# Performance work log

Hardware: AMD Instinct MI355X
Metric: run time of the kernel (lower is better)

## Reference

```python
import jax, jax.numpy as jnp
import numpy as np

D = 64
H = 4
FF = 4  # fourier features
EPS = 1e-5


def _ln(x, g, b):
    m = jnp.mean(x, axis=-1, keepdims=True)
    v = jnp.mean((x - m) ** 2, axis=-1, keepdims=True)
    return (x - m) / jnp.sqrt(v + EPS) * g + b


def setup_inputs() -> dict:
    key = jax.random.key(0)
    ks = jax.random.split(key, 30)
    s = 0.05
    inp = {
        'feats': jax.random.normal(ks[0], (1, 1024, D), jnp.float32),
        'coors': jax.random.normal(ks[1], (1, 1024, 3), jnp.float32),
        'qkv_w': jax.random.normal(ks[2], (D, 3 * D), jnp.float32) * s,
        'out_w': jax.random.normal(ks[3], (D, D), jnp.float32) * s,
        'out_b': jnp.zeros((D,), jnp.float32),
        'edge_w1': jax.random.normal(ks[4], (2 * FF + 1, D), jnp.float32) * s,
        'edge_b1': jnp.zeros((D,), jnp.float32),
        'edge_w2': jax.random.normal(ks[5], (D, D), jnp.float32) * s,
        'edge_b2': jnp.zeros((D,), jnp.float32),
        'coord_w1': jax.random.normal(ks[6], (D, D), jnp.float32) * s,
        'coord_b1': jnp.zeros((D,), jnp.float32),
        'coord_w2': jax.random.normal(ks[7], (D, 1), jnp.float32) * s,
        'coord_b2': jnp.zeros((1,), jnp.float32),
        'gate_w1': jax.random.normal(ks[8], (D, D), jnp.float32) * s,
        'gate_b1': jnp.zeros((D,), jnp.float32),
        'gate_w2': jax.random.normal(ks[9], (D, 1), jnp.float32) * s,
        'gate_b2': jnp.zeros((1,), jnp.float32),
        'ln1_g': jnp.ones((D,), jnp.float32),
        'ln1_b': jnp.zeros((D,), jnp.float32),
        'ln2_g': jnp.ones((D,), jnp.float32),
        'ln2_b': jnp.zeros((D,), jnp.float32),
        'ffn_w1': jax.random.normal(ks[10], (D, 4 * D), jnp.float32) * s,
        'ffn_b1': jnp.zeros((4 * D,), jnp.float32),
        'ffn_w2': jax.random.normal(ks[11], (4 * D, D), jnp.float32) * s,
        'ffn_b2': jnp.zeros((D,), jnp.float32),
    }
    return inp


def reference(feats, coors, qkv_w, out_w, out_b, edge_w1, edge_b1, edge_w2, edge_b2,
              coord_w1, coord_b1, coord_w2, coord_b2, gate_w1, gate_b1, gate_w2, gate_b2,
              ln1_g, ln1_b, ln2_g, ln2_b, ffn_w1, ffn_b1, ffn_w2, ffn_b2):
    B, N, Dm = feats.shape
    x = _ln(feats, ln1_g, ln1_b)  # norm1 (pre-norm; also used as residual base, faithful to source)

    # pairwise relative coords and squared distance
    rel = coors[:, :, None, :] - coors[:, None, :, :]        # [B,N,N,3]
    rd = jnp.sum(rel ** 2, axis=-1, keepdims=True)            # [B,N,N,1]
    freqs = 2.0 ** jnp.arange(FF, dtype=coors.dtype)
    fr = rd / freqs                                           # [B,N,N,FF]
    enc = jnp.concatenate([jnp.sin(fr), jnp.cos(fr), rd], -1) # [B,N,N,2*FF+1]

    # edge MLP (edges=None, edge_dim=0)
    e_ij = jax.nn.silu(enc @ edge_w1 + edge_b1) @ edge_w2 + edge_b2  # [B,N,N,D]

    # attention
    qkv = x @ qkv_w
    q, k, v = jnp.split(qkv, 3, axis=-1)
    hd = Dm // H
    q = q.reshape(B, N, H, hd).transpose(0, 2, 1, 3)
    k = k.reshape(B, N, H, hd).transpose(0, 2, 1, 3)
    v = v.reshape(B, N, H, hd).transpose(0, 2, 1, 3)
    scores = jnp.einsum('bhid,bhjd->bhij', q, k) / jnp.sqrt(jnp.asarray(Dm, q.dtype))
    attn = jax.nn.softmax(scores, axis=-1)                    # [B,H,N,N]
    msg = jnp.einsum('bhij,bhjd->bhid', attn, v)
    msg = msg.transpose(0, 2, 1, 3).reshape(B, N, Dm)
    x = x + (msg @ out_w + out_b)
    x = x + (jax.nn.gelu(_ln(x, ln2_g, ln2_b) @ ffn_w1 + ffn_b1, approximate=False) @ ffn_w2 + ffn_b2)

    # coordinate update
    cw = (jax.nn.silu(e_ij @ coord_w1 + coord_b1) @ coord_w2 + coord_b2)[..., 0]  # [B,N,N]
    cw = cw * jnp.mean(attn, axis=1)
    gate = jax.nn.sigmoid(jax.nn.silu(x @ gate_w1 + gate_b1) @ gate_w2 + gate_b2)  # [B,N,1]
    delta = jnp.einsum('bij,bijd->bid', cw, rel) * gate
    return x, coors + delta
```

## Files before the change

kernel.cpp:

```cpp
#include <hip/hip_runtime.h>
#include <hip/hip_bf16.h>

#define N 1024
#define D 64

typedef __attribute__((ext_vector_type(8))) short bf16x8;
typedef __attribute__((ext_vector_type(4))) float f32x4;

__device__ __forceinline__ unsigned short f2b(float v) {
  unsigned u = __float_as_uint(v);
  u += 0x7fffu + ((u >> 16) & 1u);
  return (unsigned short)(u >> 16);
}
__device__ __forceinline__ unsigned short f2bc(float v) {
  union { __hip_bfloat16 h; unsigned short u; } r;
  r.h = __float2bfloat16(v);
  return r.u;
}
__device__ __forceinline__ unsigned pk2(float a, float b) {
  union { __hip_bfloat162 h; unsigned u; } r;
  r.h = __hip_bfloat162(__float2bfloat16(a), __float2bfloat16(b));
  return r.u;
}
__device__ __forceinline__ float bu(unsigned short u) {
  return __uint_as_float(((unsigned)u) << 16);
}
__device__ __forceinline__ float silu_f(float x) {
  return x * __builtin_amdgcn_rcpf(1.f + __expf(-x));
}
__device__ __forceinline__ float sigm_f(float x) {
  return __builtin_amdgcn_rcpf(1.f + __expf(-x));
}

__global__ __launch_bounds__(64) void k_ln1_qkv(
    const float* __restrict__ feats, const float* __restrict__ g, const float* __restrict__ b,
    const float* __restrict__ qkv_w, float* __restrict__ xn, float* __restrict__ qkv) {
  const int i = blockIdx.x, t = threadIdx.x;
  float v = feats[i * D + t];
  float s = v;
#pragma unroll
  for (int off = 32; off; off >>= 1) s += __shfl_xor(s, off);
  const float m = s * (1.0f / 64.0f);
  const float dv = v - m;
  float vs = dv * dv;
#pragma unroll
  for (int off = 32; off; off >>= 1) vs += __shfl_xor(vs, off);
  const float var = vs * (1.0f / 64.0f);
  const float xv = dv * rsqrtf(var + 1e-5f) * g[t] + b[t];
  xn[i * D + t] = xv;
  __shared__ float xs[D];
  xs[t] = xv;
  __syncthreads();
#pragma unroll
  for (int c = 0; c < 3; ++c) {
    const int col = t + c * 64;
    float acc = 0.f;
#pragma unroll 8
    for (int k = 0; k < D; ++k) acc += xs[k] * qkv_w[k * 192 + col];
    qkv[i * 192 + col] = acc;
  }
}

__global__ __launch_bounds__(256) void k_scores(
    const float* __restrict__ qkv, unsigned short* __restrict__ P,
    float* __restrict__ l_ws, float* __restrict__ pv_ws) {
  const int i0 = blockIdx.x * 64, j0 = blockIdx.y * 64, jb = blockIdx.y;
  const int t = threadIdx.x;
  const int lane = t & 63, h = t >> 6;
  const int l15 = lane & 15, lg = lane >> 4;
  const int r7 = l15 & 7;

  __shared__ __align__(16) unsigned short Qs[64 * 64];
  __shared__ __align__(16) unsigned short Ks[64 * 64];
  __shared__ __align__(16) unsigned short VTs[4 * 16 * 64];
  __shared__ __align__(16) unsigned short Ps[4 * 64 * 64];

  {
    const int si = t >> 2, q4 = t & 3;
    const int g0 = ((q4 * 2) ^ (si & 7)) * 8, g1 = ((q4 * 2 + 1) ^ (si & 7)) * 8;
    {
      const float* qr = &qkv[(i0 + si) * 192 + q4 * 16];
      float4 a0 = *(const float4*)(qr + 0), a1 = *(const float4*)(qr + 4);
      float4 a2 = *(const float4*)(qr + 8), a3 = *(const float4*)(qr + 12);
      *(uint4*)&Qs[si * 64 + g0] = make_uint4(
          pk2(a0.x * 0.125f, a0.y * 0.125f), pk2(a0.z * 0.125f, a0.w * 0.125f),
          pk2(a1.x * 0.125f, a1.y * 0.125f), pk2(a1.z * 0.125f, a1.w * 0.125f));
      *(uint4*)&Qs[si * 64 + g1] = make_uint4(
          pk2(a2.x * 0.125f, a2.y * 0.125f), pk2(a2.z * 0.125f, a2.w * 0.125f),
          pk2(a3.x * 0.125f, a3.y * 0.125f), pk2(a3.z * 0.125f, a3.w * 0.125f));
    }
    {
      const float* kr = &qkv[(j0 + si) * 192 + 64 + q4 * 16];
      float4 a0 = *(const float4*)(kr + 0), a1 = *(const float4*)(kr + 4);
      float4 a2 = *(const float4*)(kr + 8), a3 = *(const float4*)(kr + 12);
      *(uint4*)&Ks[si * 64 + g0] = make_uint4(pk2(a0.x, a0.y), pk2(a0.z, a0.w),
                                              pk2(a1.x, a1.y), pk2(a1.z, a1.w));
      *(uint4*)&Ks[si * 64 + g1] = make_uint4(pk2(a2.x, a2.y), pk2(a2.z, a2.w),
                                              pk2(a3.x, a3.y), pk2(a3.z, a3.w));
    }
    {
      const float* vr = &qkv[(j0 + si) * 192 + 128 + q4 * 16];
      float4 v0 = *(const float4*)(vr + 0), v1 = *(const float4*)(vr + 4);
      float4 v2 = *(const float4*)(vr + 8), v3 = *(const float4*)(vr + 12);
      float vv[16] = {v0.x, v0.y, v0.z, v0.w, v1.x, v1.y, v1.z, v1.w,
                      v2.x, v2.y, v2.z, v2.w, v3.x, v3.y, v3.z, v3.w};
      const int sj3 = si >> 3, sj7 = si & 7;
#pragma unroll
      for (int cc = 0; cc < 16; ++cc)
        VTs[q4 * 1024 + cc * 64 + ((sj3 ^ (cc & 7)) * 8) + sj7] = f2bc(vv[cc]);
    }
  }
  __syncthreads();

  const bf16x8 z8 = {0, 0, 0, 0, 0, 0, 0, 0};
  const int gk = ((h * 2 + (lg & 1)) ^ r7) * 8;
  bf16x8 qa[4], kb[4];
#pragma unroll
  for (int it = 0; it < 4; ++it) {
    qa[it] = *(const bf16x8*)&Qs[(it * 16 + l15) * 64 + gk];
    if (lg >= 2) qa[it] = z8;
    kb[it] = *(const bf16x8*)&Ks[(it * 16 + l15) * 64 + gk];
  }
  f32x4 acc[4][4];
#pragma unroll
  for (int it = 0; it < 4; ++it)
#pragma unroll
    for (int jt = 0; jt < 4; ++jt)
      acc[it][jt] = (f32x4){0.f, 0.f, 0.f, 0.f};
#pragma unroll
  for (int it = 0; it < 4; ++it)
#pragma unroll
    for (int jt = 0; jt < 4; ++jt)
      acc[it][jt] = __builtin_amdgcn_mfma_f32_16x16x32_bf16(qa[it], kb[jt], acc[it][jt], 0, 0, 0);

  float prow[4][4];
#pragma unroll
  for (int it = 0; it < 4; ++it)
#pragma unroll
    for (int rr = 0; rr < 4; ++rr) prow[it][rr] = 0.f;
#pragma unroll
  for (int it = 0; it < 4; ++it)
#pragma unroll
    for (int jt = 0; jt < 4; ++jt)
#pragma unroll
      for (int rr = 0; rr < 4; ++rr) {
        const float p = __expf(acc[it][jt][rr]);
        prow[it][rr] += p;
        const int irow = it * 16 + lg * 4 + rr;
        const int col = jt * 16 + l15;
        Ps[h * 4096 + irow * 64 + (((col >> 3) ^ (irow & 7)) * 8) + (col & 7)] = f2bc(p);
      }
#pragma unroll
  for (int it = 0; it < 4; ++it)
#pragma unroll
    for (int rr = 0; rr < 4; ++rr) {
      float s = prow[it][rr];
      s += __shfl_xor(s, 1); s += __shfl_xor(s, 2);
      s += __shfl_xor(s, 4); s += __shfl_xor(s, 8);
      if (l15 == 0)
        l_ws[h * 16384 + jb * 1024 + i0 + it * 16 + lg * 4 + rr] = s;
    }

  f32x4 av[4];
#pragma unroll
  for (int it = 0; it < 4; ++it) av[it] = (f32x4){0.f, 0.f, 0.f, 0.f};
#pragma unroll
  for (int ks = 0; ks < 2; ++ks) {
    const int gj = ((ks * 4 + lg) ^ r7) * 8;
    bf16x8 vb = *(const bf16x8*)&VTs[h * 1024 + l15 * 64 + gj];
#pragma unroll
    for (int it = 0; it < 4; ++it) {
      bf16x8 pa = *(const bf16x8*)&Ps[h * 4096 + (it * 16 + l15) * 64 + gj];
      av[it] = __builtin_amdgcn_mfma_f32_16x16x32_bf16(pa, vb, av[it], 0, 0, 0);
    }
  }
#pragma unroll
  for (int it = 0; it < 4; ++it)
#pragma unroll
    for (int rr = 0; rr < 4; ++rr)
      pv_ws[jb * 65536 + (i0 + it * 16 + lg * 4 + rr) * 64 + h * 16 + l15] = av[it][rr];

  {
    const int ir = t & 63;
    unsigned short* pg = &P[h * 1048576 + (i0 + ir) * 1024 + j0];
#pragma unroll
    for (int gg = 0; gg < 8; ++gg)
      *(uint4*)&pg[gg * 8] = *(const uint4*)&Ps[h * 4096 + ir * 64 + ((gg ^ (ir & 7)) * 8)];
  }
}

__global__ __launch_bounds__(256) void k_meanattn(
    const unsigned short* P, const float* __restrict__ l_ws,
    unsigned short* ma, unsigned short* __restrict__ maT) {
  const int i0 = blockIdx.x * 64, j0 = blockIdx.y * 64;
  const int t = threadIdx.x;
  __shared__ float invl[4][64];
  __shared__ unsigned short tile[64][68];
  {
    const int h = t >> 6, r = t & 63;
    float s = 0.f;
#pragma unroll
    for (int jt = 0; jt < 16; ++jt) s += l_ws[h * 16384 + jt * 1024 + i0 + r];
    invl[h][r] = 0.25f * __builtin_amdgcn_rcpf(s);
  }
  __syncthreads();
  {
    const int r = t >> 2, cg = t & 3;
    float v[16];
#pragma unroll
    for (int k = 0; k < 16; ++k) v[k] = 0.f;
#pragma unroll
    for (int h = 0; h < 4; ++h) {
      const unsigned short* pr = &P[h * 1048576 + (i0 + r) * 1024 + j0 + cg * 16];
      uint4 a = *(const uint4*)pr;
      uint4 b2 = *(const uint4*)(pr + 8);
      const float sh = invl[h][r];
      unsigned uu[8] = {a.x, a.y, a.z, a.w, b2.x, b2.y, b2.z, b2.w};
#pragma unroll
      for (int q = 0; q < 8; ++q) {
        v[q * 2 + 0] += sh * bu((unsigned short)(uu[q] & 0xffffu));
        v[q * 2 + 1] += sh * bu((unsigned short)(uu[q] >> 16));
      }
    }
    unsigned out[8];
#pragma unroll
    for (int q = 0; q < 8; ++q) out[q] = pk2(v[2 * q], v[2 * q + 1]);
    unsigned short* mr = &ma[(i0 + r) * 1024 + j0 + cg * 16];
    *(uint4*)mr = make_uint4(out[0], out[1], out[2], out[3]);
    *(uint4*)(mr + 8) = make_uint4(out[4], out[5], out[6], out[7]);
#pragma unroll
    for (int q = 0; q < 8; ++q) {
      tile[r][cg * 16 + 2 * q] = (unsigned short)(out[q] & 0xffffu);
      tile[r][cg * 16 + 2 * q + 1] = (unsigned short)(out[q] >> 16);
    }
  }
  __syncthreads();
  {
    const int jr = t >> 2, icg = t & 3;
    unsigned out[8];
#pragma unroll
    for (int q = 0; q < 8; ++q) {
      const unsigned short lo = tile[icg * 16 + 2 * q][jr];
      const unsigned short hi = tile[icg * 16 + 2 * q + 1][jr];
      out[q] = (unsigned)lo | ((unsigned)hi << 16);
    }
    unsigned short* mtr = &maT[(j0 + jr) * 1024 + i0 + icg * 16];
    *(uint4*)mtr = make_uint4(out[0], out[1], out[2], out[3]);
    *(uint4*)(mtr + 8) = make_uint4(out[4], out[5], out[6], out[7]);
  }
}

__global__ __launch_bounds__(256) void k_ffn_gate(
    const float* __restrict__ pv_ws, const float* __restrict__ l_ws,
    const float* __restrict__ xn,
    const float* __restrict__ out_w, const float* __restrict__ out_b,
    const float* __restrict__ ln2_g, const float* __restrict__ ln2_b,
    const float* __restrict__ fw1, const float* __restrict__ fb1,
    const float* __restrict__ fw2, const float* __restrict__ fb2,
    const float* __restrict__ gw1, const float* __restrict__ gb1,
    const float* __restrict__ gw2, const float* __restrict__ gb2,
    float* __restrict__ xout, float* __restrict__ gate) {
  const int i = blockIdx.x, t = threadIdx.x;
  __shared__ float msgv[64], xs[64], x1s[64], hs[256];
  if (t < 64) {
    float ls = 0.f;
#pragma unroll
    for (int jt = 0; jt < 16; ++jt) ls += l_ws[(t >> 4) * 16384 + jt * 1024 + i];
    const float invh = __builtin_amdgcn_rcpf(ls);
    float s = 0.f;
#pragma unroll
    for (int jt = 0; jt < 16; ++jt) s += pv_ws[jt * 65536 + i * 64 + t];
    msgv[t] = s * invh;
  }
  __syncthreads();
  if (t < 64) {
    float o = out_b[t];
#pragma unroll 8
    for (int k = 0; k < 64; ++k) o += msgv[k] * out_w[k * 64 + t];
    const float v = xn[i * 64 + t] + o;
    x1s[t] = v;
    float s = v;
#pragma unroll
    for (int off = 32; off; off >>= 1) s += __shfl_xor(s, off);
    const float m = s * (1.f / 64.f);
    const float dv = v - m;
    float vs = dv * dv;
#pragma unroll
    for (int off = 32; off; off >>= 1) vs += __shfl_xor(vs, off);
    xs[t] = dv * rsqrtf(vs * (1.f / 64.f) + 1e-5f) * ln2_g[t] + ln2_b[t];
  }
  __syncthreads();
  float a = fb1[t];
#pragma unroll 8
  for (int k = 0; k < 64; ++k) a += xs[k] * fw1[k * 256 + t];
  const float ge = 0.5f * a * (1.f + erff(a * 0.70710678118f));
  hs[t] = ge;
  __syncthreads();
  if (t < 64) {
    float o = fb2[t];
#pragma unroll 8
    for (int k = 0; k < 256; ++k) o += hs[k] * fw2[k * 64 + t];
    const float xo = x1s[t] + o;
    xout[i * 64 + t] = xo;
    xs[t] = xo;
  }
  __syncthreads();
  if (t < 64) {
    float a2 = gb1[t];
#pragma unroll 8
    for (int k = 0; k < 64; ++k) a2 += xs[k] * gw1[k * 64 + t];
    const float sg = a2 * sigm_f(a2);
    float pp = sg * gw2[t];
#pragma unroll
    for (int off = 32; off; off >>= 1) pp += __shfl_xor(pp, off);
    if (t == 0) gate[i] = sigm_f(pp + gb2[0]);
  }
}

__global__ __launch_bounds__(256) void k_prep(
    const float* __restrict__ ew1, const float* __restrict__ eb1,
    const float* __restrict__ ew2, const float* __restrict__ cw1,
    const float* __restrict__ eb2, const float* __restrict__ cb1,
    unsigned short* __restrict__ pw, float* __restrict__ b3p) {
  const int t = threadIdx.x;
  __shared__ float wc[64][64];
  for (int idx = t; idx < 4096; idx += 256) {
    const int r = idx >> 6, c = idx & 63;
    float s = 0.f;
#pragma unroll 8
    for (int k = 0; k < 64; ++k) s += ew2[r * 64 + k] * cw1[k * 64 + c];
    wc[r][c] = s;
  }
  __syncthreads();
  for (int idx = t; idx < 12 * 512; idx += 256) {
    const int e = idx & 7, l = (idx >> 3) & 63, f = idx >> 9;
    const int l15 = l & 15, lg = l >> 4;
    float v;
    if (f < 4) {
      const int d = f * 16 + l15, k = lg * 8 + e;
      v = (k < 9) ? ew1[k * 64 + d] : (k == 9 ? eb1[d] : 0.f);
    } else {
      const int g = f - 4, d = (g >> 1) * 16 + l15, k = (g & 1) * 32 + lg * 8 + e;
      v = wc[k][d];
    }
    pw[idx] = f2b(v);
  }
  if (t < 64) {
    float s = cb1[t];
#pragma unroll 8
    for (int k = 0; k < 64; ++k) s += eb2[k] * cw1[k * 64 + t];
    b3p[t] = s;
  }
}

__global__ __launch_bounds__(256, 2) void k_pair(
    const float* __restrict__ coors,
    const unsigned short* __restrict__ ma, const unsigned short* __restrict__ maT,
    const unsigned short* __restrict__ pw,
    const float* __restrict__ b3p, const float* __restrict__ c2g,
    const float* __restrict__ cb2, float* __restrict__ partial) {
  int bb = blockIdx.x, ti = 0;
  while (bb >= 32 - ti) { bb -= 32 - ti; ++ti; }
  const int tj = ti + bb;
  const bool diag = (ti == tj);
  const int nch = diag ? 4 : 8;

  const int t = threadIdx.x;
  const int w = t >> 6;
  const int lane = t & 63;
  const int l15 = lane & 15;
  const int lg = lane >> 4;

  __shared__ __align__(16) unsigned short buf[4][32][64];
  __shared__ float4 relA[4][32], relB[4][32];
  __shared__ float di[4][32][3], dj[4][32][3];

  bf16x8 wf[12];
#pragma unroll
  for (int f = 0; f < 12; ++f)
    wf[f] = *(const bf16x8*)&pw[(f * 64 + lane) * 8];

  float b3v[16], c2v[16];
#pragma unroll
  for (int mt = 0; mt < 4; ++mt)
#pragma unroll
    for (int r = 0; r < 4; ++r) {
      const int d = mt * 16 + lg * 4 + r;
      b3v[mt * 4 + r] = b3p[d];
      c2v[mt * 4 + r] = c2g[d];
    }
  const float cb2q = cb2[0] * 0.25f;

  if (lane < 32) {
    const int j = lane;
#pragma unroll
    for (int k2 = 0; k2 < 3; ++k2) { di[w][j][k2] = 0.f; dj[w][j][k2] = 0.f; }
    unsigned short* rp = &buf[w][j][0];
    const uint4 z4 = make_uint4(0, 0, 0, 0);
    *(uint4*)&rp[(1 ^ (j & 7)) * 8] = z4;
    *(uint4*)&rp[(2 ^ (j & 7)) * 8] = z4;
    *(uint4*)&rp[(3 ^ (j & 7)) * 8] = z4;
  }

  f32x4 acc[4][2];

  for (int c = 0; c < nch; ++c) {
    const int dgn = diag ? (c * 4 + w + 1) : (c * 4 + w);
    {
      const int p = lane & 31;
      const int hhalf = lane >> 5;
      const int ig = ti * 32 + p;
      const int jj = (p + dgn) & 31;
      const int jg = tj * 32 + jj;
      const float rx = coors[ig * 3 + 0] - coors[jg * 3 + 0];
      const float ry = coors[ig * 3 + 1] - coors[jg * 3 + 1];
      const float rz = coors[ig * 3 + 2] - coors[jg * 3 + 2];
      const float rd = rx * rx + ry * ry + rz * rz;
      unsigned short* rp = &buf[w][p][0];
      if (hhalf == 0) {
        float mi = bu(ma[ig * 1024 + jg]);
        float mj = bu(maT[ig * 1024 + jg]);
        if (diag && dgn == 16 && p >= 16) { mi = 0.f; mj = 0.f; }
        relA[w][p] = make_float4(mi * rx, mi * ry, mi * rz, 0.f);
        relB[w][p] = make_float4(mj * rx, mj * ry, mj * rz, 0.f);
        *(uint2*)&rp[(0 ^ (p & 7)) * 8] =
            make_uint2(pk2(__sinf(rd), __sinf(rd * 0.5f)),
                       pk2(__sinf(rd * 0.25f), __sinf(rd * 0.125f)));
        *(unsigned*)&rp[(1 ^ (p & 7)) * 8] = pk2(rd, 1.0f);
      } else {
        *(uint2*)&rp[((0 ^ (p & 7)) * 8) + 4] =
            make_uint2(pk2(__cosf(rd), __cosf(rd * 0.5f)),
                       pk2(__cosf(rd * 0.25f), __cosf(rd * 0.125f)));
      }
    }

#pragma unroll
    for (int mt = 0; mt < 4; ++mt)
#pragma unroll
      for (int nt = 0; nt < 2; ++nt)
        acc[mt][nt] = (f32x4){0.f, 0.f, 0.f, 0.f};
    {
      const int j0 = l15, j1 = 16 + l15;
      bf16x8 bf0 = *(const bf16x8*)&buf[w][j0][(lg ^ (j0 & 7)) * 8];
      bf16x8 bf1 = *(const bf16x8*)&buf[w][j1][(lg ^ (j1 & 7)) * 8];
#pragma unroll
      for (int mt = 0; mt < 4; ++mt) {
        acc[mt][0] = __builtin_amdgcn_mfma_f32_16x16x32_bf16(wf[mt], bf0, acc[mt][0], 0, 0, 0);
        acc[mt][1] = __builtin_amdgcn_mfma_f32_16x16x32_bf16(wf[mt], bf1, acc[mt][1], 0, 0, 0);
      }
    }
#pragma unroll
    for (int mt = 0; mt < 4; ++mt)
#pragma unroll
      for (int nt = 0; nt < 2; ++nt) {
        const f32x4 a = acc[mt][nt];
        const unsigned lo = pk2(silu_f(a[0]), silu_f(a[1]));
        const unsigned hi = pk2(silu_f(a[2]), silu_f(a[3]));
        const int j = nt * 16 + l15;
        const int g = mt * 2 + (lg >> 1);
        *(uint2*)&buf[w][j][((g ^ (j & 7)) * 8) + (lg & 1) * 4] = make_uint2(lo, hi);
      }

#pragma unroll
    for (int mt = 0; mt < 4; ++mt)
#pragma unroll
      for (int nt = 0; nt < 2; ++nt)
        acc[mt][nt] = (f32x4){b3v[mt * 4 + 0], b3v[mt * 4 + 1], b3v[mt * 4 + 2], b3v[mt * 4 + 3]};
#pragma unroll
    for (int ks = 0; ks < 2; ++ks) {
      const int gi = ks * 4 + lg;
      const int j0 = l15, j1 = 16 + l15;
      bf16x8 bf0 = *(const bf16x8*)&buf[w][j0][(gi ^ (j0 & 7)) * 8];
      bf16x8 bf1 = *(const bf16x8*)&buf[w][j1][(gi ^ (j1 & 7)) * 8];
#pragma unroll
      for (int mt = 0; mt < 4; ++mt) {
        acc[mt][0] = __builtin_amdgcn_mfma_f32_16x16x32_bf16(wf[4 + mt * 2 + ks], bf0, acc[mt][0], 0, 0, 0);
        acc[mt][1] = __builtin_amdgcn_mfma_f32_16x16x32_bf16(wf[4 + mt * 2 + ks], bf1, acc[mt][1], 0, 0, 0);
      }
    }

#pragma unroll
    for (int nt = 0; nt < 2; ++nt) {
      float cwp = cb2q;
#pragma unroll
      for (int mt = 0; mt < 4; ++mt) {
        const f32x4 a = acc[mt][nt];
#pragma unroll
        for (int r = 0; r < 4; ++r) cwp += silu_f(a[r]) * c2v[mt * 4 + r];
      }
      cwp += __shfl_xor(cwp, 16);
      cwp += __shfl_xor(cwp, 32);
      if (lg == 0) {
        const int p = nt * 16 + l15;
        const int jj = (p + dgn) & 31;
        const float4 rA = relA[w][p];
        const float4 rB = relB[w][p];
        di[w][p][0] += cwp * rA.x; di[w][p][1] += cwp * rA.y; di[w][p][2] += cwp * rA.z;
        dj[w][jj][0] -= cwp * rB.x; dj[w][jj][1] -= cwp * rB.y; dj[w][jj][2] -= cwp * rB.z;
      }
    }
  }

  __syncthreads();
  if (!diag) {
    if (t < 96) {
      const int p = t / 3, k = t % 3;
      const float s = di[0][p][k] + di[1][p][k] + di[2][p][k] + di[3][p][k];
      partial[tj * 3072 + (ti * 32 + p) * 3 + k] = s;
    } else if (t < 192) {
      const int u = t - 96, q = u / 3, k = u % 3;
      const float s = dj[0][q][k] + dj[1][q][k] + dj[2][q][k] + dj[3][q][k];
      partial[ti * 3072 + (tj * 32 + q) * 3 + k] = s;
    }
  } else {
    if (t < 96) {
      const int p = t / 3, k = t % 3;
      const float s = di[0][p][k] + di[1][p][k] + di[2][p][k] + di[3][p][k]
                    + dj[0][p][k] + dj[1][p][k] + dj[2][p][k] + dj[3][p][k];
      partial[ti * 3072 + (ti * 32 + p) * 3 + k] = s;
    }
  }
}

__global__ __launch_bounds__(256) void k_finalize(
    const float* __restrict__ coors, const float* __restrict__ partial,
    const float* __restrict__ gate, float* __restrict__ outc) {
  const int idx = blockIdx.x * 256 + threadIdx.x;
  if (idx < 3072) {
    float s = 0.f;
#pragma unroll
    for (int sl = 0; sl < 32; ++sl) s += partial[sl * 3072 + idx];
    outc[idx] = coors[idx] + s * gate[idx / 3];
  }
}

extern "C" void kernel_launch(void* const* d_in, const int* in_sizes, int n_in,
                              void* d_out, int out_size, void* d_ws, size_t ws_size,
                              hipStream_t stream) {
  const float* feats = (const float*)d_in[0];
  const float* coors = (const float*)d_in[1];
  const float* qkv_w = (const float*)d_in[2];
  const float* out_w = (const float*)d_in[3];
  const float* out_b = (const float*)d_in[4];
  const float* ew1 = (const float*)d_in[5];
  const float* eb1 = (const float*)d_in[6];
  const float* ew2 = (const float*)d_in[7];
  const float* eb2 = (const float*)d_in[8];
  const float* cw1 = (const float*)d_in[9];
  const float* cb1 = (const float*)d_in[10];
  const float* cw2 = (const float*)d_in[11];
  const float* cb2 = (const float*)d_in[12];
  const float* gw1 = (const float*)d_in[13];
  const float* gb1 = (const float*)d_in[14];
  const float* gw2 = (const float*)d_in[15];
  const float* gb2 = (const float*)d_in[16];
  const float* ln1_g = (const float*)d_in[17];
  const float* ln1_b = (const float*)d_in[18];
  const float* ln2_g = (const float*)d_in[19];
  const float* ln2_b = (const float*)d_in[20];
  const float* fw1 = (const float*)d_in[21];
  const float* fb1 = (const float*)d_in[22];
  const float* fw2 = (const float*)d_in[23];
  const float* fb2 = (const float*)d_in[24];

  float* ws = (float*)d_ws;
  float* xn = ws;
  float* qkv = ws + 65536;
  float* gate = ws + 262144;
  unsigned short* pw = (unsigned short*)(ws + 263168);
  float* b3p = ws + 266240;
  float* l_ws = ws + 266304;
  float* pv_ws = ws + 331840;
  float* partial = ws + 1380416;
  unsigned short* P = (unsigned short*)(ws + 1478720);
  unsigned short* ma = P;
  unsigned short* maT = (unsigned short*)(ws + 3575872);

  float* xout = (float*)d_out;
  float* coorout = xout + 65536;

  hipLaunchKernelGGL(k_ln1_qkv, dim3(N), dim3(64), 0, stream, feats, ln1_g, ln1_b, qkv_w, xn, qkv);
  hipLaunchKernelGGL(k_prep, dim3(1), dim3(256), 0, stream, ew1, eb1, ew2, cw1, eb2, cb1, pw, b3p);
  hipLaunchKernelGGL(k_scores, dim3(16, 16), dim3(256), 0, stream, qkv, P, l_ws, pv_ws);
  hipLaunchKernelGGL(k_meanattn, dim3(16, 16), dim3(256), 0, stream, P, l_ws, ma, maT);
  hipLaunchKernelGGL(k_ffn_gate, dim3(N), dim3(256), 0, stream, pv_ws, l_ws, xn,
                     out_w, out_b, ln2_g, ln2_b,
                     fw1, fb1, fw2, fb2, gw1, gb1, gw2, gb2, xout, gate);
  hipLaunchKernelGGL(k_pair, dim3(528), dim3(256), 0, stream, coors, ma, maT, pw,
                     b3p, cw2, cb2, partial);
  hipLaunchKernelGGL(k_finalize, dim3(12), dim3(256), 0, stream, coors, partial, gate, coorout);
}
```

Before: 105.2 us.

## Drop transposed mean-attention buffer and shrink pair tiles to 16x16

Removes the maT transpose output from k_meanattn, eliminating its shared-memory tile, a barrier and a full N×N bf16 write. k_pair now reads the transposed entry directly from ma at [jg, ig], which is a strided, uncoalesced gather. The pair kernel's triangular tiling changes from 32-row tiles (528 blocks) to 16-row tiles (2080 blocks) with fewer diagonal iterations per block, so finalize now sums 64 partial slices. The finer grid improves load balance and occupancy, at the cost of more per-block setup such as weight fragment loads and zeroing.

```diff
diff --git a/kernel.cpp b/kernel.cpp
--- a/kernel.cpp
+++ b/kernel.cpp
@@ -190,12 +190,10 @@
 }
 
 __global__ __launch_bounds__(256) void k_meanattn(
-    const unsigned short* P, const float* __restrict__ l_ws,
-    unsigned short* ma, unsigned short* __restrict__ maT) {
+    const unsigned short* P, const float* __restrict__ l_ws, unsigned short* ma) {
   const int i0 = blockIdx.x * 64, j0 = blockIdx.y * 64;
   const int t = threadIdx.x;
   __shared__ float invl[4][64];
-  __shared__ unsigned short tile[64][68];
   {
     const int h = t >> 6, r = t & 63;
     float s = 0.f;
@@ -228,25 +226,6 @@
     unsigned short* mr = &ma[(i0 + r) * 1024 + j0 + cg * 16];
     *(uint4*)mr = make_uint4(out[0], out[1], out[2], out[3]);
     *(uint4*)(mr + 8) = make_uint4(out[4], out[5], out[6], out[7]);
-#pragma unroll
-    for (int q = 0; q < 8; ++q) {
-      tile[r][cg * 16 + 2 * q] = (unsigned short)(out[q] & 0xffffu);
-      tile[r][cg * 16 + 2 * q + 1] = (unsigned short)(out[q] >> 16);
-    }
-  }
-  __syncthreads();
-  {
-    const int jr = t >> 2, icg = t & 3;
-    unsigned out[8];
-#pragma unroll
-    for (int q = 0; q < 8; ++q) {
-      const unsigned short lo = tile[icg * 16 + 2 * q][jr];
-      const unsigned short hi = tile[icg * 16 + 2 * q + 1][jr];
-      out[q] = (unsigned)lo | ((unsigned)hi << 16);
-    }
-    unsigned short* mtr = &maT[(j0 + jr) * 1024 + i0 + icg * 16];
-    *(uint4*)mtr = make_uint4(out[0], out[1], out[2], out[3]);
-    *(uint4*)(mtr + 8) = make_uint4(out[4], out[5], out[6], out[7]);
   }
 }
 
@@ -354,16 +333,15 @@
 }
 
 __global__ __launch_bounds__(256, 2) void k_pair(
-    const float* __restrict__ coors,
-    const unsigned short* __restrict__ ma, const unsigned short* __restrict__ maT,
+    const float* __restrict__ coors, const unsigned short* __restrict__ ma,
     const unsigned short* __restrict__ pw,
     const float* __restrict__ b3p, const float* __restrict__ c2g,
     const float* __restrict__ cb2, float* __restrict__ partial) {
   int bb = blockIdx.x, ti = 0;
-  while (bb >= 32 - ti) { bb -= 32 - ti; ++ti; }
+  while (bb >= 64 - ti) { bb -= 64 - ti; ++ti; }
   const int tj = ti + bb;
   const bool diag = (ti == tj);
-  const int nch = diag ? 4 : 8;
+  const int niter = diag ? 1 : 2;
 
   const int t = threadIdx.x;
   const int w = t >> 6;
@@ -373,7 +351,7 @@
 
   __shared__ __align__(16) unsigned short buf[4][32][64];
   __shared__ float4 relA[4][32], relB[4][32];
-  __shared__ float di[4][32][3], dj[4][32][3];
+  __shared__ float di[4][16][3], dj[4][16][3];
 
   bf16x8 wf[12];
 #pragma unroll
@@ -393,42 +371,45 @@
 
   if (lane < 32) {
     const int j = lane;
-#pragma unroll
-    for (int k2 = 0; k2 < 3; ++k2) { di[w][j][k2] = 0.f; dj[w][j][k2] = 0.f; }
     unsigned short* rp = &buf[w][j][0];
     const uint4 z4 = make_uint4(0, 0, 0, 0);
     *(uint4*)&rp[(1 ^ (j & 7)) * 8] = z4;
     *(uint4*)&rp[(2 ^ (j & 7)) * 8] = z4;
     *(uint4*)&rp[(3 ^ (j & 7)) * 8] = z4;
   }
+  if (lane < 16) {
+#pragma unroll
+    for (int k2 = 0; k2 < 3; ++k2) { di[w][lane][k2] = 0.f; dj[w][lane][k2] = 0.f; }
+  }
 
   f32x4 acc[4][2];
 
-  for (int c = 0; c < nch; ++c) {
-    const int dgn = diag ? (c * 4 + w + 1) : (c * 4 + w);
+  for (int c = 0; c < niter; ++c) {
+    const int d0 = diag ? (1 + w * 2) : ((w + c * 4) * 2);
     {
-      const int p = lane & 31;
+      const int cc = lane & 31;
       const int hhalf = lane >> 5;
-      const int ig = ti * 32 + p;
-      const int jj = (p + dgn) & 31;
-      const int jg = tj * 32 + jj;
+      const int p = cc & 15;
+      const int dd = d0 + (cc >> 4);
+      const int ig = ti * 16 + p;
+      const int jg = tj * 16 + ((p + dd) & 15);
       const float rx = coors[ig * 3 + 0] - coors[jg * 3 + 0];
       const float ry = coors[ig * 3 + 1] - coors[jg * 3 + 1];
       const float rz = coors[ig * 3 + 2] - coors[jg * 3 + 2];
       const float rd = rx * rx + ry * ry + rz * rz;
-      unsigned short* rp = &buf[w][p][0];
+      unsigned short* rp = &buf[w][cc][0];
       if (hhalf == 0) {
         float mi = bu(ma[ig * 1024 + jg]);
-        float mj = bu(maT[ig * 1024 + jg]);
-        if (diag && dgn == 16 && p >= 16) { mi = 0.f; mj = 0.f; }
-        relA[w][p] = make_float4(mi * rx, mi * ry, mi * rz, 0.f);
-        relB[w][p] = make_float4(mj * rx, mj * ry, mj * rz, 0.f);
-        *(uint2*)&rp[(0 ^ (p & 7)) * 8] =
+        float mj = bu(ma[jg * 1024 + ig]);
+        if (diag && dd == 8 && p >= 8) { mi = 0.f; mj = 0.f; }
+        relA[w][cc] = make_float4(mi * rx, mi * ry, mi * rz, 0.f);
+        relB[w][cc] = make_float4(mj * rx, mj * ry, mj * rz, 0.f);
+        *(uint2*)&rp[(0 ^ (cc & 7)) * 8] =
             make_uint2(pk2(__sinf(rd), __sinf(rd * 0.5f)),
                        pk2(__sinf(rd * 0.25f), __sinf(rd * 0.125f)));
-        *(unsigned*)&rp[(1 ^ (p & 7)) * 8] = pk2(rd, 1.0f);
+        *(unsigned*)&rp[(1 ^ (cc & 7)) * 8] = pk2(rd, 1.0f);
       } else {
-        *(uint2*)&rp[((0 ^ (p & 7)) * 8) + 4] =
+        *(uint2*)&rp[((0 ^ (cc & 7)) * 8) + 4] =
             make_uint2(pk2(__cosf(rd), __cosf(rd * 0.5f)),
                        pk2(__cosf(rd * 0.25f), __cosf(rd * 0.125f)));
       }
@@ -491,10 +472,12 @@
       cwp += __shfl_xor(cwp, 16);
       cwp += __shfl_xor(cwp, 32);
       if (lg == 0) {
-        const int p = nt * 16 + l15;
-        const int jj = (p + dgn) & 31;
-        const float4 rA = relA[w][p];
-        const float4 rB = relB[w][p];
+        const int cc = nt * 16 + l15;
+        const int p = l15;
+        const int dd = d0 + nt;
+        const int jj = (p + dd) & 15;
+        const float4 rA = relA[w][cc];
+        const float4 rB = relB[w][cc];
         di[w][p][0] += cwp * rA.x; di[w][p][1] += cwp * rA.y; di[w][p][2] += cwp * rA.z;
         dj[w][jj][0] -= cwp * rB.x; dj[w][jj][1] -= cwp * rB.y; dj[w][jj][2] -= cwp * rB.z;
       }
@@ -503,21 +486,21 @@
 
   __syncthreads();
   if (!diag) {
-    if (t < 96) {
+    if (t < 48) {
       const int p = t / 3, k = t % 3;
       const float s = di[0][p][k] + di[1][p][k] + di[2][p][k] + di[3][p][k];
-      partial[tj * 3072 + (ti * 32 + p) * 3 + k] = s;
-    } else if (t < 192) {
-      const int u = t - 96, q = u / 3, k = u % 3;
+      partial[tj * 3072 + (ti * 16 + p) * 3 + k] = s;
+    } else if (t < 96) {
+      const int u = t - 48, q = u / 3, k = u % 3;
       const float s = dj[0][q][k] + dj[1][q][k] + dj[2][q][k] + dj[3][q][k];
-      partial[ti * 3072 + (tj * 32 + q) * 3 + k] = s;
+      partial[ti * 3072 + (tj * 16 + q) * 3 + k] = s;
     }
   } else {
-    if (t < 96) {
+    if (t < 48) {
       const int p = t / 3, k = t % 3;
       const float s = di[0][p][k] + di[1][p][k] + di[2][p][k] + di[3][p][k]
                     + dj[0][p][k] + dj[1][p][k] + dj[2][p][k] + dj[3][p][k];
-      partial[ti * 3072 + (ti * 32 + p) * 3 + k] = s;
+      partial[ti * 3072 + (ti * 16 + p) * 3 + k] = s;
     }
   }
 }
@@ -529,7 +512,7 @@
   if (idx < 3072) {
     float s = 0.f;
 #pragma unroll
-    for (int sl = 0; sl < 32; ++sl) s += partial[sl * 3072 + idx];
+    for (int sl = 0; sl < 64; ++sl) s += partial[sl * 3072 + idx];
     outc[idx] = coors[idx] + s * gate[idx / 3];
   }
 }
@@ -572,9 +555,8 @@
   float* l_ws = ws + 266304;
   float* pv_ws = ws + 331840;
   float* partial = ws + 1380416;
-  unsigned short* P = (unsigned short*)(ws + 1478720);
+  unsigned short* P = (unsigned short*)(ws + 1577024);
   unsigned short* ma = P;
-  unsigned short* maT = (unsigned short*)(ws + 3575872);
 
   float* xout = (float*)d_out;
   float* coorout = xout + 65536;
@@ -582,11 +564,11 @@
   hipLaunchKernelGGL(k_ln1_qkv, dim3(N), dim3(64), 0, stream, feats, ln1_g, ln1_b, qkv_w, xn, qkv);
   hipLaunchKernelGGL(k_prep, dim3(1), dim3(256), 0, stream, ew1, eb1, ew2, cw1, eb2, cb1, pw, b3p);
   hipLaunchKernelGGL(k_scores, dim3(16, 16), dim3(256), 0, stream, qkv, P, l_ws, pv_ws);
-  hipLaunchKernelGGL(k_meanattn, dim3(16, 16), dim3(256), 0, stream, P, l_ws, ma, maT);
+  hipLaunchKernelGGL(k_meanattn, dim3(16, 16), dim3(256), 0, stream, P, l_ws, ma);
   hipLaunchKernelGGL(k_ffn_gate, dim3(N), dim3(256), 0, stream, pv_ws, l_ws, xn,
                      out_w, out_b, ln2_g, ln2_b,
                      fw1, fb1, fw2, fb2, gw1, gb1, gw2, gb2, xout, gate);
-  hipLaunchKernelGGL(k_pair, dim3(528), dim3(256), 0, stream, coors, ma, maT, pw,
+  hipLaunchKernelGGL(k_pair, dim3(2080), dim3(256), 0, stream, coors, ma, pw,
                      b3p, cw2, cb2, partial);
   hipLaunchKernelGGL(k_finalize, dim3(12), dim3(256), 0, stream, coors, partial, gate, coorout);
 }
```

Result: slower. 111.8 us (+6.2%).

## Merge prep into LN/QKV kernel, drop transposed mean-attn, widen pair blocks

Applied to the files above, without the earlier changes.

The weight-prep kernel is folded into the LN1+QKV kernel as an extra block, and LN1+QKV now handles four rows per 256-thread block, which removes one launch. The transposed mean-attention matrix is no longer written; k_pair reads ma with transposed indexing instead, which saves a write pass but makes those loads strided. k_pair now runs with 512 threads (8 waves) that each do fewer iterations. The cb2 scaling changes from cb2*0.25 to cb2, presumably because the work split per block changed, which carries a correctness risk.

```diff
diff --git a/kernel.cpp b/kernel.cpp
--- a/kernel.cpp
+++ b/kernel.cpp
@@ -32,11 +32,49 @@
   return __builtin_amdgcn_rcpf(1.f + __expf(-x));
 }
 
-__global__ __launch_bounds__(64) void k_ln1_qkv(
+__global__ __launch_bounds__(256) void k_ln1_qkv_prep(
     const float* __restrict__ feats, const float* __restrict__ g, const float* __restrict__ b,
-    const float* __restrict__ qkv_w, float* __restrict__ xn, float* __restrict__ qkv) {
-  const int i = blockIdx.x, t = threadIdx.x;
-  float v = feats[i * D + t];
+    const float* __restrict__ qkv_w, float* __restrict__ xn, float* __restrict__ qkv,
+    const float* __restrict__ ew1, const float* __restrict__ eb1,
+    const float* __restrict__ ew2, const float* __restrict__ cw1,
+    const float* __restrict__ eb2, const float* __restrict__ cb1,
+    unsigned short* __restrict__ pw, float* __restrict__ b3p) {
+  __shared__ float sh[64 * 64];
+  const int t = threadIdx.x;
+  if (blockIdx.x == 256) {
+    float* wc = sh;
+    for (int idx = t; idx < 4096; idx += 256) {
+      const int r = idx >> 6, c = idx & 63;
+      float s = 0.f;
+#pragma unroll 8
+      for (int k = 0; k < 64; ++k) s += ew2[r * 64 + k] * cw1[k * 64 + c];
+      wc[idx] = s;
+    }
+    __syncthreads();
+    for (int idx = t; idx < 12 * 512; idx += 256) {
+      const int e = idx & 7, l = (idx >> 3) & 63, f = idx >> 9;
+      const int l15 = l & 15, lg = l >> 4;
+      float v;
+      if (f < 4) {
+        const int d = f * 16 + l15, k = lg * 8 + e;
+        v = (k < 9) ? ew1[k * 64 + d] : (k == 9 ? eb1[d] : 0.f);
+      } else {
+        const int gq = f - 4, d = (gq >> 1) * 16 + l15, k = (gq & 1) * 32 + lg * 8 + e;
+        v = wc[k * 64 + d];
+      }
+      pw[idx] = f2b(v);
+    }
+    if (t < 64) {
+      float s = cb1[t];
+#pragma unroll 8
+      for (int k = 0; k < 64; ++k) s += eb2[k] * cw1[k * 64 + t];
+      b3p[t] = s;
+    }
+    return;
+  }
+  const int r = t >> 6, lane = t & 63;
+  const int i = blockIdx.x * 4 + r;
+  float v = feats[i * D + lane];
   float s = v;
 #pragma unroll
   for (int off = 32; off; off >>= 1) s += __shfl_xor(s, off);
@@ -46,17 +84,17 @@
 #pragma unroll
   for (int off = 32; off; off >>= 1) vs += __shfl_xor(vs, off);
   const float var = vs * (1.0f / 64.0f);
-  const float xv = dv * rsqrtf(var + 1e-5f) * g[t] + b[t];
-  xn[i * D + t] = xv;
-  __shared__ float xs[D];
-  xs[t] = xv;
+  const float xv = dv * rsqrtf(var + 1e-5f) * g[lane] + b[lane];
+  xn[i * D + lane] = xv;
+  float* xs = sh;
+  xs[r * 64 + lane] = xv;
   __syncthreads();
 #pragma unroll
   for (int c = 0; c < 3; ++c) {
-    const int col = t + c * 64;
+    const int col = lane + c * 64;
     float acc = 0.f;
 #pragma unroll 8
-    for (int k = 0; k < D; ++k) acc += xs[k] * qkv_w[k * 192 + col];
+    for (int k = 0; k < D; ++k) acc += xs[r * 64 + k] * qkv_w[k * 192 + col];
     qkv[i * 192 + col] = acc;
   }
 }
@@ -190,12 +228,10 @@
 }
 
 __global__ __launch_bounds__(256) void k_meanattn(
-    const unsigned short* P, const float* __restrict__ l_ws,
-    unsigned short* ma, unsigned short* __restrict__ maT) {
+    const unsigned short* P, const float* __restrict__ l_ws, unsigned short* ma) {
   const int i0 = blockIdx.x * 64, j0 = blockIdx.y * 64;
   const int t = threadIdx.x;
   __shared__ float invl[4][64];
-  __shared__ unsigned short tile[64][68];
   {
     const int h = t >> 6, r = t & 63;
     float s = 0.f;
@@ -228,25 +264,6 @@
     unsigned short* mr = &ma[(i0 + r) * 1024 + j0 + cg * 16];
     *(uint4*)mr = make_uint4(out[0], out[1], out[2], out[3]);
     *(uint4*)(mr + 8) = make_uint4(out[4], out[5], out[6], out[7]);
-#pragma unroll
-    for (int q = 0; q < 8; ++q) {
-      tile[r][cg * 16 + 2 * q] = (unsigned short)(out[q] & 0xffffu);
-      tile[r][cg * 16 + 2 * q + 1] = (unsigned short)(out[q] >> 16);
-    }
-  }
-  __syncthreads();
-  {
-    const int jr = t >> 2, icg = t & 3;
-    unsigned out[8];
-#pragma unroll
-    for (int q = 0; q < 8; ++q) {
-      const unsigned short lo = tile[icg * 16 + 2 * q][jr];
-      const unsigned short hi = tile[icg * 16 + 2 * q + 1][jr];
-      out[q] = (unsigned)lo | ((unsigned)hi << 16);
-    }
-    unsigned short* mtr = &maT[(j0 + jr) * 1024 + i0 + icg * 16];
-    *(uint4*)mtr = make_uint4(out[0], out[1], out[2], out[3]);
-    *(uint4*)(mtr + 8) = make_uint4(out[4], out[5], out[6], out[7]);
   }
 }
 
@@ -317,45 +334,8 @@
   }
 }
 
-__global__ __launch_bounds__(256) void k_prep(
-    const float* __restrict__ ew1, const float* __restrict__ eb1,
-    const float* __restrict__ ew2, const float* __restrict__ cw1,
-    const float* __restrict__ eb2, const float* __restrict__ cb1,
-    unsigned short* __restrict__ pw, float* __restrict__ b3p) {
-  const int t = threadIdx.x;
-  __shared__ float wc[64][64];
-  for (int idx = t; idx < 4096; idx += 256) {
-    const int r = idx >> 6, c = idx & 63;
-    float s = 0.f;
-#pragma unroll 8
-    for (int k = 0; k < 64; ++k) s += ew2[r * 64 + k] * cw1[k * 64 + c];
-    wc[r][c] = s;
-  }
-  __syncthreads();
-  for (int idx = t; idx < 12 * 512; idx += 256) {
-    const int e = idx & 7, l = (idx >> 3) & 63, f = idx >> 9;
-    const int l15 = l & 15, lg = l >> 4;
-    float v;
-    if (f < 4) {
-      const int d = f * 16 + l15, k = lg * 8 + e;
-      v = (k < 9) ? ew1[k * 64 + d] : (k == 9 ? eb1[d] : 0.f);
-    } else {
-      const int g = f - 4, d = (g >> 1) * 16 + l15, k = (g & 1) * 32 + lg * 8 + e;
-      v = wc[k][d];
-    }
-    pw[idx] = f2b(v);
-  }
-  if (t < 64) {
-    float s = cb1[t];
-#pragma unroll 8
-    for (int k = 0; k < 64; ++k) s += eb2[k] * cw1[k * 64 + t];
-    b3p[t] = s;
-  }
-}
-
-__global__ __launch_bounds__(256, 2) void k_pair(
-    const float* __restrict__ coors,
-    const unsigned short* __restrict__ ma, const unsigned short* __restrict__ maT,
+__global__ __launch_bounds__(512) void k_pair(
+    const float* __restrict__ coors, const unsigned short* __restrict__ ma,
     const unsigned short* __restrict__ pw,
     const float* __restrict__ b3p, const float* __restrict__ c2g,
     const float* __restrict__ cb2, float* __restrict__ partial) {
@@ -363,7 +343,7 @@
   while (bb >= 32 - ti) { bb -= 32 - ti; ++ti; }
   const int tj = ti + bb;
   const bool diag = (ti == tj);
-  const int nch = diag ? 4 : 8;
+  const int niter = diag ? 2 : 4;
 
   const int t = threadIdx.x;
   const int w = t >> 6;
@@ -371,9 +351,9 @@
   const int l15 = lane & 15;
   const int lg = lane >> 4;
 
-  __shared__ __align__(16) unsigned short buf[4][32][64];
-  __shared__ float4 relA[4][32], relB[4][32];
-  __shared__ float di[4][32][3], dj[4][32][3];
+  __shared__ __align__(16) unsigned short buf[8][32][64];
+  __shared__ float4 relA[8][32], relB[8][32];
+  __shared__ float di[8][32][3], dj[8][32][3];
 
   bf16x8 wf[12];
 #pragma unroll
@@ -389,8 +369,7 @@
       b3v[mt * 4 + r] = b3p[d];
       c2v[mt * 4 + r] = c2g[d];
     }
-  const float cb2q = cb2[0] * 0.25f;
-
+  const float cb2q = cb2[0];
   if (lane < 32) {
     const int j = lane;
 #pragma unroll
@@ -404,8 +383,8 @@
 
   f32x4 acc[4][2];
 
-  for (int c = 0; c < nch; ++c) {
-    const int dgn = diag ? (c * 4 + w + 1) : (c * 4 + w);
+  for (int c = 0; c < niter; ++c) {
+    const int dgn = diag ? (c * 8 + w + 1) : (c * 8 + w);
     {
       const int p = lane & 31;
       const int hhalf = lane >> 5;
@@ -419,7 +398,7 @@
       unsigned short* rp = &buf[w][p][0];
       if (hhalf == 0) {
         float mi = bu(ma[ig * 1024 + jg]);
-        float mj = bu(maT[ig * 1024 + jg]);
+        float mj = bu(ma[jg * 1024 + ig]);
         if (diag && dgn == 16 && p >= 16) { mi = 0.f; mj = 0.f; }
         relA[w][p] = make_float4(mi * rx, mi * ry, mi * rz, 0.f);
         relB[w][p] = make_float4(mj * rx, mj * ry, mj * rz, 0.f);
@@ -505,18 +484,23 @@
   if (!diag) {
     if (t < 96) {
       const int p = t / 3, k = t % 3;
-      const float s = di[0][p][k] + di[1][p][k] + di[2][p][k] + di[3][p][k];
+      float s = 0.f;
+#pragma unroll
+      for (int q = 0; q < 8; ++q) s += di[q][p][k];
       partial[tj * 3072 + (ti * 32 + p) * 3 + k] = s;
     } else if (t < 192) {
-      const int u = t - 96, q = u / 3, k = u % 3;
-      const float s = dj[0][q][k] + dj[1][q][k] + dj[2][q][k] + dj[3][q][k];
-      partial[ti * 3072 + (tj * 32 + q) * 3 + k] = s;
+      const int u = t - 96, q2 = u / 3, k = u % 3;
+      float s = 0.f;
+#pragma unroll
+      for (int q = 0; q < 8; ++q) s += dj[q][q2][k];
+      partial[ti * 3072 + (tj * 32 + q2) * 3 + k] = s;
     }
   } else {
     if (t < 96) {
       const int p = t / 3, k = t % 3;
-      const float s = di[0][p][k] + di[1][p][k] + di[2][p][k] + di[3][p][k]
-                    + dj[0][p][k] + dj[1][p][k] + dj[2][p][k] + dj[3][p][k];
+      float s = 0.f;
+#pragma unroll
+      for (int q = 0; q < 8; ++q) s += di[q][p][k] + dj[q][p][k];
       partial[ti * 3072 + (ti * 32 + p) * 3 + k] = s;
     }
   }
@@ -574,19 +558,19 @@
   float* partial = ws + 1380416;
   unsigned short* P = (unsigned short*)(ws + 1478720);
   unsigned short* ma = P;
-  unsigned short* maT = (unsigned short*)(ws + 3575872);
 
   float* xout = (float*)d_out;
   float* coorout = xout + 65536;
 
-  hipLaunchKernelGGL(k_ln1_qkv, dim3(N), dim3(64), 0, stream, feats, ln1_g, ln1_b, qkv_w, xn, qkv);
-  hipLaunchKernelGGL(k_prep, dim3(1), dim3(256), 0, stream, ew1, eb1, ew2, cw1, eb2, cb1, pw, b3p);
+  hipLaunchKernelGGL(k_ln1_qkv_prep, dim3(257), dim3(256), 0, stream,
+                     feats, ln1_g, ln1_b, qkv_w, xn, qkv,
+                     ew1, eb1, ew2, cw1, eb2, cb1, pw, b3p);
   hipLaunchKernelGGL(k_scores, dim3(16, 16), dim3(256), 0, stream, qkv, P, l_ws, pv_ws);
-  hipLaunchKernelGGL(k_meanattn, dim3(16, 16), dim3(256), 0, stream, P, l_ws, ma, maT);
+  hipLaunchKernelGGL(k_meanattn, dim3(16, 16), dim3(256), 0, stream, P, l_ws, ma);
   hipLaunchKernelGGL(k_ffn_gate, dim3(N), dim3(256), 0, stream, pv_ws, l_ws, xn,
                      out_w, out_b, ln2_g, ln2_b,
                      fw1, fb1, fw2, fb2, gw1, gb1, gw2, gb2, xout, gate);
-  hipLaunchKernelGGL(k_pair, dim3(528), dim3(256), 0, stream, coors, ma, maT, pw,
+  hipLaunchKernelGGL(k_pair, dim3(528), dim3(512), 0, stream, coors, ma, pw,
                      b3p, cw2, cb2, partial);
   hipLaunchKernelGGL(k_finalize, dim3(12), dim3(256), 0, stream, coors, partial, gate, coorout);
 }
```

New measurement: 108.5 us. 1.03x slower.
